# Optimization experiments

Hardware: AMD Instinct MI355X
Metric: run time of the kernel (lower is better)

The kernel has to match this reference:

```python
import math
import jax, jax.numpy as jnp
import numpy as np

IN_DIM = 512
OUT_DIM = 512
K = 3
EPS = 1e-8


def setup_inputs() -> dict:
    key = jax.random.key(0)
    k1, k2, k3 = jax.random.split(key, 3)
    b, h, w = 8, 64, 64
    x = jax.random.normal(k1, (b, IN_DIM, h, w), dtype=jnp.float32)
    style = jax.random.normal(k2, (b, IN_DIM), dtype=jnp.float32)
    weight = jax.random.normal(k3, (OUT_DIM, IN_DIM, K, K), dtype=jnp.float32)
    bias = jnp.zeros((OUT_DIM,), dtype=jnp.float32)
    return {"x": x, "style": style, "weight": weight, "bias": bias}


def _mod_weights(weight, style):
    # EqualizedWeight scaling: c = 1/sqrt(prod(shape[1:]))
    c = 1.0 / math.sqrt(IN_DIM * K * K)
    w = weight * c                                    # [out, in, k, k]
    ws = w[None] * (style[:, None, :, None, None] + 1.0)  # [b, out, in, k, k]
    sigma_inv = jax.lax.rsqrt(jnp.sum(ws * ws, axis=(2, 3, 4), keepdims=True) + EPS)
    return ws * sigma_inv


def reference(x, style, weight, bias):
    ws = _mod_weights(weight, style)                  # [b, out, in, k, k]

    def conv_one(xi, wi):
        # xi: [in, h, w], wi: [out, in, k, k]
        y = jax.lax.conv_general_dilated(
            xi[None], wi, window_strides=(1, 1), padding="SAME",
            dimension_numbers=("NCHW", "OIHW", "NCHW"))
        return y[0]

    out = jax.vmap(conv_one)(x, ws)                   # [b, out, h, w]
    return out + bias[None, :, None, None]
```

## Files before the change

### kernel.cpp

```cpp
#include <hip/hip_runtime.h>

#define CIN 512
#define COUT 512
#define HH 64
#define WW 64
#define BB 8
#define KTOT 4608

#define XPD 66
#define BUFSH (4 * 66 * 64)
#define ROWB (66 * 128)

typedef __attribute__((ext_vector_type(8))) short short8;
typedef __attribute__((ext_vector_type(4))) float f32x4;

__device__ inline unsigned short f2bf(float f) {
    unsigned int u = __float_as_uint(f);
    u += 0x7FFFu + ((u >> 16) & 1u);
    return (unsigned short)(u >> 16);
}

__device__ inline void gll16(const void* g, void* l) {
    __builtin_amdgcn_global_load_lds(
        (const __attribute__((address_space(1))) unsigned int*)g,
        (__attribute__((address_space(3))) unsigned int*)l, 16, 0, 0);
}

__global__ __launch_bounds__(256) void zring_kernel(unsigned short* __restrict__ xtp) {
    const int e = blockIdx.x * 256 + threadIdx.x;
    if (e >= BB * 260 * 64) return;
    const int unit = e & 63;
    const int sa = e >> 6;
    const int b = sa / 260;
    const int s = sa - b * 260;
    int yy, xx;
    if (s < 66)       { yy = 0;        xx = s; }
    else if (s < 132) { yy = 65;       xx = s - 66; }
    else if (s < 196) { yy = s - 131;  xx = 0; }
    else              { yy = s - 195;  xx = 65; }
    *(short8*)(xtp + ((size_t)(b * XPD + yy) * XPD + xx) * 512 + unit * 8) =
        (short8){0, 0, 0, 0, 0, 0, 0, 0};
}

__global__ __launch_bounds__(256) void xpose_kernel(const float* __restrict__ x,
                                                    const float* __restrict__ style,
                                                    unsigned short* __restrict__ xtp) {
    __shared__ float tile[32 * 65];
    __shared__ float sst[32];
    const int ic = blockIdx.x;
    const int y  = blockIdx.y;
    const int b  = blockIdx.z;
    const int t  = threadIdx.x;
    if (t < 32) sst[t] = style[b * CIN + ic * 32 + t] + 1.0f;
#pragma unroll
    for (int it = 0; it < 8; ++it) {
        int e = it * 256 + t;
        int ii = e >> 6, xx = e & 63;
        tile[ii * 65 + xx] = x[(((size_t)(b * CIN + ic * 32 + ii) * HH + y) << 6) + xx];
    }
    __syncthreads();
#pragma unroll
    for (int it = 0; it < 8; ++it) {
        int g = it * 256 + t;
        int xx = g >> 5, ii = g & 31;
        xtp[((size_t)(b * XPD + y + 1) * XPD + xx + 1) * 512 + ic * 32 + ii] =
            f2bf(tile[ii * 65 + xx] * sst[ii]);
    }
}

__global__ __launch_bounds__(256) void wpack_kernel(const float* __restrict__ weight,
                                                    unsigned short* __restrict__ wpk) {
    __shared__ float q[KTOT];
    const int o = blockIdx.x;
    const int t = threadIdx.x;
    const float* wrow = weight + (size_t)o * KTOT;
    const float cst = 1.0f / sqrtf((float)KTOT);
#pragma unroll
    for (int it = 0; it < 18; ++it) {
        int e = it * 256 + t;
        q[e] = wrow[e] * cst;
    }
    __syncthreads();
    const int g = o >> 4, l15 = o & 15;
    for (int m = t; m < 576; m += 256) {
        int c   = m / 36;
        int rem = m - c * 36;
        int tap = rem >> 2;
        int l4  = rem & 3;
        short8 v;
#pragma unroll
        for (int e = 0; e < 8; ++e)
            v[e] = (short)f2bf(q[(c * 32 + l4 * 8 + e) * 9 + tap]);
        *(short8*)(wpk + ((((size_t)c * 9 + tap) * 32 + g) * 64 + l4 * 16 + l15) * 8) = v;
    }
}

__global__ __launch_bounds__(256) void sigma_kernel(const float* __restrict__ weight,
                                                    const float* __restrict__ style,
                                                    float* __restrict__ siginv) {
    __shared__ float sred[4][8];
    const int o = blockIdx.x;
    const int t = threadIdx.x;
    const float* wrow = weight + (size_t)o * KTOT;
    float acc[8] = {0.f, 0.f, 0.f, 0.f, 0.f, 0.f, 0.f, 0.f};
#pragma unroll
    for (int ii = 0; ii < 2; ++ii) {
        const int i = t * 2 + ii;
        float wsq = 0.f;
#pragma unroll
        for (int tap = 0; tap < 9; ++tap) {
            float v = wrow[i * 9 + tap];
            wsq += v * v;
        }
#pragma unroll
        for (int b = 0; b < 8; ++b) {
            float s = style[b * CIN + i] + 1.0f;
            acc[b] += wsq * s * s;
        }
    }
#pragma unroll
    for (int b = 0; b < 8; ++b) {
        float v = acc[b];
#pragma unroll
        for (int off = 32; off > 0; off >>= 1) v += __shfl_down(v, off, 64);
        if ((t & 63) == 0) sred[t >> 6][b] = v;
    }
    __syncthreads();
    if (t < 8) {
        const float S = sred[0][t] + sred[1][t] + sred[2][t] + sred[3][t];
        siginv[t * COUT + o] = rsqrtf(S * (1.0f / (float)KTOT) + 1e-8f);
    }
}

__global__ __launch_bounds__(512, 4) void conv_kernel(const unsigned short* __restrict__ wpk,
                                                      const unsigned short* __restrict__ xtp,
                                                      const float* __restrict__ siginv,
                                                      const float* __restrict__ bias,
                                                      float* __restrict__ out) {
    __shared__ __align__(16) unsigned short xs[2 * BUFSH];
    const int bid = blockIdx.x;
    const int k  = bid & 7;
    const int tq = bid >> 3;
    const int ob = k & 1;
    const int b  = (k >> 1) * 2 + (tq >> 5);
    const int yb = tq & 31;
    const int y0 = yb * 2;

    const int tid  = threadIdx.x;
    const int lane = tid & 63;
    const int wid_u = __builtin_amdgcn_readfirstlane(tid >> 6);
    const int l15 = lane & 15, l4 = lane >> 4;
    const int og = wid_u & 3, rp = wid_u >> 2;
    const int g0 = ob * 16 + og * 4;

    const int up = lane & 7;
    const unsigned short* srcq[4];
#pragma unroll
    for (int t4 = 0; t4 < 4; ++t4) {
        const int sl = (wid_u + t4 * 8) * 8 + (lane >> 3);
        const int row = sl / 66, col = sl - row * 66;
        srcq[t4] = xtp + ((size_t)(b * XPD + y0 + row) * XPD + col) * 512 +
                   (up ^ (col & 7)) * 8;
    }
    const int col4 = 58 + (lane >> 3);
    const unsigned short* src4 =
        xtp + ((size_t)(b * XPD + y0 + 3) * XPD + col4) * 512 + (up ^ (col4 & 7)) * 8;

    int vB[3][2];
#pragma unroll
    for (int kx = 0; kx < 3; ++kx)
#pragma unroll
        for (int ks = 0; ks < 2; ++ks)
            vB[kx][ks] = (l15 + kx) * 128 + (((ks * 4 + l4) ^ ((l15 + kx) & 7)) * 16);

    f32x4 acc[4][4];
#pragma unroll
    for (int mi = 0; mi < 4; ++mi)
#pragma unroll
        for (int j = 0; j < 4; ++j) acc[mi][j] = (f32x4){0.f, 0.f, 0.f, 0.f};

    const unsigned short* wB = wpk + (size_t)g0 * 512 + lane * 8;

#define STAGE(bufp, icq)                                                                  \
    do {                                                                                  \
        unsigned short* dbase = xs + (bufp) * BUFSH + wid_u * 512;                        \
        gll16(srcq[0] + (size_t)(icq) * 64, dbase);                                       \
        gll16(srcq[1] + (size_t)(icq) * 64, dbase + 4096);                                \
        gll16(srcq[2] + (size_t)(icq) * 64, dbase + 8192);                                \
        gll16(srcq[3] + (size_t)(icq) * 64, dbase + 12288);                               \
        if (wid_u == 0)                                                                   \
            gll16(src4 + (size_t)(icq) * 64, xs + (bufp) * BUFSH + 16384);                \
    } while (0)

#define PHASE(tap, ks, wAc, cbase)                                                        \
    do {                                                                                  \
        short8 afx[4];                                                                    \
        _Pragma("unroll") for (int mi = 0; mi < 4; ++mi)                                  \
            afx[mi] = *(const short8*)((wAc) + ((ks) * 9 + (tap)) * 16384 + mi * 512);    \
        short8 bfr[4];                                                                    \
        const char* bp = (const char*)xs + (cbase) +                                      \
                         (rp + (tap) / 3) * ROWB + vB[(tap) % 3][ks];                     \
        _Pragma("unroll") for (int j = 0; j < 4; ++j)                                     \
            bfr[j] = *(const short8*)(bp + j * 2048);                                     \
        __builtin_amdgcn_s_setprio(1);                                                    \
        _Pragma("unroll") for (int mi = 0; mi < 4; ++mi)                                  \
            _Pragma("unroll") for (int j = 0; j < 4; ++j)                                 \
                acc[mi][j] = __builtin_amdgcn_mfma_f32_16x16x32_bf16(                     \
                    afx[mi], bfr[j], acc[mi][j], 0, 0, 0);                                \
        __builtin_amdgcn_s_setprio(0);                                                    \
    } while (0)

    STAGE(0, 0);
    __syncthreads();

#pragma unroll 1
    for (int ic = 0; ic < 8; ++ic) {
        if (ic < 7) STAGE((ic + 1) & 1, ic + 1);
        const unsigned short* wAc = wB + (size_t)ic * (2 * 9 * 32 * 512);
        const int cbase = (ic & 1) * (BUFSH * 2);
#pragma unroll
        for (int tap = 0; tap < 9; ++tap) {
            PHASE(tap, 0, wAc, cbase);
            PHASE(tap, 1, wAc, cbase);
        }
        __syncthreads();
    }

    const int yout = y0 + rp;
#pragma unroll
    for (int mi = 0; mi < 4; ++mi) {
        const int obase = ob * 256 + og * 64 + mi * 16 + l4 * 4;
#pragma unroll
        for (int rr = 0; rr < 4; ++rr) {
            const int o = obase + rr;
            const float sv = siginv[b * COUT + o];
            const float bv = bias[o];
            float* orow = out + (((size_t)(b * COUT + o) * HH + yout) << 6);
#pragma unroll
            for (int j = 0; j < 4; ++j) {
                orow[j * 16 + l15] = acc[mi][j][rr] * sv + bv;
            }
        }
    }
#undef STAGE
#undef PHASE
}

extern "C" void kernel_launch(void* const* d_in, const int* in_sizes, int n_in,
                              void* d_out, int out_size, void* d_ws, size_t ws_size,
                              hipStream_t stream) {
    const float* x      = (const float*)d_in[0];
    const float* style  = (const float*)d_in[1];
    const float* weight = (const float*)d_in[2];
    const float* bias   = (const float*)d_in[3];
    float* out = (float*)d_out;

    unsigned short* wpk = (unsigned short*)d_ws;
    unsigned short* xtp = wpk + (size_t)2359296;
    float* siginv = (float*)(xtp + (size_t)BB * XPD * XPD * 512);

    zring_kernel<<<520, 256, 0, stream>>>(xtp);
    xpose_kernel<<<dim3(16, HH, BB), 256, 0, stream>>>(x, style, xtp);
    wpack_kernel<<<COUT, 256, 0, stream>>>(weight, wpk);
    sigma_kernel<<<COUT, 256, 0, stream>>>(weight, style, siginv);
    conv_kernel<<<512, 512, 0, stream>>>(wpk, xtp, siginv, bias, out);
}
```

Baseline: 165.9 us.

## Shrink conv tile to one output row per block and prefetch weights two steps ahead

Each conv block now computes one output row with 4 waves instead of two rows with 8 waves. Grid size doubles to 1024 blocks and the LDS halo stage drops from 4 input rows to 3. Weight fragments are loaded into a 3-deep register ring, so A-operand global loads are issued two MFMA phases before use, hiding their latency. The trade-off is that each input row is staged 3 times instead of 2, adding LDS and global traffic. The extra register ring may also limit occupancy.

```diff
diff --git a/kernel.cpp b/kernel.cpp
--- a/kernel.cpp
+++ b/kernel.cpp
@@ -8,7 +8,7 @@
 #define KTOT 4608
 
 #define XPD 66
-#define BUFSH (4 * 66 * 64)
+#define BUFSH (3 * 66 * 64)
 #define ROWB (66 * 128)
 
 typedef __attribute__((ext_vector_type(8))) short short8;
@@ -132,7 +132,7 @@
     }
 }
 
-__global__ __launch_bounds__(512, 4) void conv_kernel(const unsigned short* __restrict__ wpk,
+__global__ __launch_bounds__(256, 3) void conv_kernel(const unsigned short* __restrict__ wpk,
                                                       const unsigned short* __restrict__ xtp,
                                                       const float* __restrict__ siginv,
                                                       const float* __restrict__ bias,
@@ -140,31 +140,30 @@
     __shared__ __align__(16) unsigned short xs[2 * BUFSH];
     const int bid = blockIdx.x;
     const int k  = bid & 7;
-    const int tq = bid >> 3;
+    const int t  = bid >> 3;
     const int ob = k & 1;
-    const int b  = (k >> 1) * 2 + (tq >> 5);
-    const int yb = tq & 31;
-    const int y0 = yb * 2;
+    const int b  = (k >> 1) * 2 + (t >> 6);
+    const int yb = t & 63;
 
     const int tid  = threadIdx.x;
     const int lane = tid & 63;
     const int wid_u = __builtin_amdgcn_readfirstlane(tid >> 6);
     const int l15 = lane & 15, l4 = lane >> 4;
-    const int og = wid_u & 3, rp = wid_u >> 2;
+    const int og = wid_u;
     const int g0 = ob * 16 + og * 4;
 
     const int up = lane & 7;
-    const unsigned short* srcq[4];
-#pragma unroll
-    for (int t4 = 0; t4 < 4; ++t4) {
-        const int sl = (wid_u + t4 * 8) * 8 + (lane >> 3);
+    const unsigned short* srcq[6];
+#pragma unroll
+    for (int tq = 0; tq < 6; ++tq) {
+        const int sl = (wid_u + tq * 4) * 8 + (lane >> 3);
         const int row = sl / 66, col = sl - row * 66;
-        srcq[t4] = xtp + ((size_t)(b * XPD + y0 + row) * XPD + col) * 512 +
+        srcq[tq] = xtp + ((size_t)(b * XPD + yb + row) * XPD + col) * 512 +
                    (up ^ (col & 7)) * 8;
     }
-    const int col4 = 58 + (lane >> 3);
-    const unsigned short* src4 =
-        xtp + ((size_t)(b * XPD + y0 + 3) * XPD + col4) * 512 + (up ^ (col4 & 7)) * 8;
+    const int col6 = 60 + (lane >> 3);
+    const unsigned short* src6 =
+        xtp + ((size_t)(b * XPD + yb + 2) * XPD + col6) * 512 + (up ^ (col6 & 7)) * 8;
 
     int vB[3][2];
 #pragma unroll
@@ -179,54 +178,63 @@
 #pragma unroll
         for (int j = 0; j < 4; ++j) acc[mi][j] = (f32x4){0.f, 0.f, 0.f, 0.f};
 
-    const unsigned short* wB = wpk + (size_t)g0 * 512 + lane * 8;
+    short8 af[3][4];
+
+    const unsigned short* aP = wpk + (size_t)g0 * 512 + lane * 8;
 
 #define STAGE(bufp, icq)                                                                  \
     do {                                                                                  \
         unsigned short* dbase = xs + (bufp) * BUFSH + wid_u * 512;                        \
-        gll16(srcq[0] + (size_t)(icq) * 64, dbase);                                       \
-        gll16(srcq[1] + (size_t)(icq) * 64, dbase + 4096);                                \
-        gll16(srcq[2] + (size_t)(icq) * 64, dbase + 8192);                                \
-        gll16(srcq[3] + (size_t)(icq) * 64, dbase + 12288);                               \
-        if (wid_u == 0)                                                                   \
-            gll16(src4 + (size_t)(icq) * 64, xs + (bufp) * BUFSH + 16384);                \
+        _Pragma("unroll") for (int tq = 0; tq < 6; ++tq)                                  \
+            gll16(srcq[tq] + (size_t)(icq) * 64, dbase + tq * 2048);                      \
+        if (wid_u == 0 && lane < 48)                                                      \
+            gll16(src6 + (size_t)(icq) * 64, xs + (bufp) * BUFSH + 12288);                \
     } while (0)
 
-#define PHASE(tap, ks, wAc, cbase)                                                        \
+#define PHASE(s, aPic, cbase)                                                             \
     do {                                                                                  \
-        short8 afx[4];                                                                    \
+        const unsigned short* pA = (aPic) + (size_t)((s) + 2) * 16384;                    \
         _Pragma("unroll") for (int mi = 0; mi < 4; ++mi)                                  \
-            afx[mi] = *(const short8*)((wAc) + ((ks) * 9 + (tap)) * 16384 + mi * 512);    \
+            af[((s) + 2) % 3][mi] = *(const short8*)(pA + mi * 512);                      \
         short8 bfr[4];                                                                    \
         const char* bp = (const char*)xs + (cbase) +                                      \
-                         (rp + (tap) / 3) * ROWB + vB[(tap) % 3][ks];                     \
+                         (((s) % 9) / 3) * ROWB + vB[((s) % 9) % 3][(s) / 9];             \
         _Pragma("unroll") for (int j = 0; j < 4; ++j)                                     \
             bfr[j] = *(const short8*)(bp + j * 2048);                                     \
         __builtin_amdgcn_s_setprio(1);                                                    \
         _Pragma("unroll") for (int mi = 0; mi < 4; ++mi)                                  \
             _Pragma("unroll") for (int j = 0; j < 4; ++j)                                 \
                 acc[mi][j] = __builtin_amdgcn_mfma_f32_16x16x32_bf16(                     \
-                    afx[mi], bfr[j], acc[mi][j], 0, 0, 0);                                \
+                    af[(s) % 3][mi], bfr[j], acc[mi][j], 0, 0, 0);                        \
         __builtin_amdgcn_s_setprio(0);                                                    \
     } while (0)
 
+    af[0][0] = *(const short8*)(aP + 0 * 512);
+    af[0][1] = *(const short8*)(aP + 1 * 512);
+    af[0][2] = *(const short8*)(aP + 2 * 512);
+    af[0][3] = *(const short8*)(aP + 3 * 512);
+    {
+        const unsigned short* p1 = aP + 16384;
+        af[1][0] = *(const short8*)(p1 + 0 * 512);
+        af[1][1] = *(const short8*)(p1 + 1 * 512);
+        af[1][2] = *(const short8*)(p1 + 2 * 512);
+        af[1][3] = *(const short8*)(p1 + 3 * 512);
+    }
     STAGE(0, 0);
     __syncthreads();
 
 #pragma unroll 1
     for (int ic = 0; ic < 8; ++ic) {
         if (ic < 7) STAGE((ic + 1) & 1, ic + 1);
-        const unsigned short* wAc = wB + (size_t)ic * (2 * 9 * 32 * 512);
+        const unsigned short* aPic = aP + (size_t)ic * (18 * 16384);
         const int cbase = (ic & 1) * (BUFSH * 2);
 #pragma unroll
-        for (int tap = 0; tap < 9; ++tap) {
-            PHASE(tap, 0, wAc, cbase);
-            PHASE(tap, 1, wAc, cbase);
+        for (int s = 0; s < 18; ++s) {
+            PHASE(s, aPic, cbase);
         }
         __syncthreads();
     }
 
-    const int yout = y0 + rp;
 #pragma unroll
     for (int mi = 0; mi < 4; ++mi) {
         const int obase = ob * 256 + og * 64 + mi * 16 + l4 * 4;
@@ -235,7 +243,7 @@
             const int o = obase + rr;
             const float sv = siginv[b * COUT + o];
             const float bv = bias[o];
-            float* orow = out + (((size_t)(b * COUT + o) * HH + yout) << 6);
+            float* orow = out + (((size_t)(b * COUT + o) * HH + yb) << 6);
 #pragma unroll
             for (int j = 0; j < 4; ++j) {
                 orow[j * 16 + l15] = acc[mi][j][rr] * sv + bv;
@@ -263,5 +271,5 @@
     xpose_kernel<<<dim3(16, HH, BB), 256, 0, stream>>>(x, style, xtp);
     wpack_kernel<<<COUT, 256, 0, stream>>>(weight, wpk);
     sigma_kernel<<<COUT, 256, 0, stream>>>(weight, style, siginv);
-    conv_kernel<<<512, 512, 0, stream>>>(wpk, xtp, siginv, bias, out);
-}
+    conv_kernel<<<1024, 256, 0, stream>>>(wpk, xtp, siginv, bias, out);
+}
```

Result: no change. 168.7 us (+1.6%).

## Enlarge conv tile to 8 rows by 128 channels with register-rotated weight prefetch

Applied to the files above, without the earlier changes.

Reshapes the conv block tile from 2 output rows × 256 output channels to 8 rows × 128 channels, with 32-channel staging chunks over 16 iterations. Each wave now holds 4×8 accumulators, and weight fragments are prefetched two taps ahead through a three-slot register rotation. The grid drops to 256 blocks at occupancy 2. The aim is more weight reuse per loaded fragment, less redundant halo loading, and hiding global weight-load latency behind MFMAs. The cost is more register pressure and only one block per CU, so less latency hiding across blocks.

```diff
diff --git a/kernel.cpp b/kernel.cpp
--- a/kernel.cpp
+++ b/kernel.cpp
@@ -8,8 +8,9 @@
 #define KTOT 4608
 
 #define XPD 66
-#define BUFSH (4 * 66 * 64)
-#define ROWB (66 * 128)
+#define BUFSH (10 * 66 * 32)
+#define BUFB  (BUFSH * 2)
+#define ROWB  (66 * 64)
 
 typedef __attribute__((ext_vector_type(8))) short short8;
 typedef __attribute__((ext_vector_type(4))) float f32x4;
@@ -132,7 +133,7 @@
     }
 }
 
-__global__ __launch_bounds__(512, 4) void conv_kernel(const unsigned short* __restrict__ wpk,
+__global__ __launch_bounds__(512, 2) void conv_kernel(const unsigned short* __restrict__ wpk,
                                                       const unsigned short* __restrict__ xtp,
                                                       const float* __restrict__ siginv,
                                                       const float* __restrict__ bias,
@@ -140,110 +141,124 @@
     __shared__ __align__(16) unsigned short xs[2 * BUFSH];
     const int bid = blockIdx.x;
     const int k  = bid & 7;
-    const int tq = bid >> 3;
-    const int ob = k & 1;
-    const int b  = (k >> 1) * 2 + (tq >> 5);
-    const int yb = tq & 31;
-    const int y0 = yb * 2;
+    const int t  = bid >> 3;
+    const int ob = k & 3;
+    const int b  = (k >> 2) * 4 + (t >> 3);
+    const int rg = t & 7;
+    const int y0r = rg * 8;
 
     const int tid  = threadIdx.x;
     const int lane = tid & 63;
     const int wid_u = __builtin_amdgcn_readfirstlane(tid >> 6);
     const int l15 = lane & 15, l4 = lane >> 4;
-    const int og = wid_u & 3, rp = wid_u >> 2;
-    const int g0 = ob * 16 + og * 4;
-
-    const int up = lane & 7;
-    const unsigned short* srcq[4];
-#pragma unroll
-    for (int t4 = 0; t4 < 4; ++t4) {
-        const int sl = (wid_u + t4 * 8) * 8 + (lane >> 3);
+    const int og = wid_u & 1, rp = wid_u >> 1;
+    const int g0 = ob * 8 + og * 4;
+
+    const int u = lane & 3;
+    const unsigned short* srcq[5];
+#pragma unroll
+    for (int t4 = 0; t4 < 5; ++t4) {
+        const int sl = (wid_u + t4 * 8) * 16 + (lane >> 2);
         const int row = sl / 66, col = sl - row * 66;
-        srcq[t4] = xtp + ((size_t)(b * XPD + y0 + row) * XPD + col) * 512 +
-                   (up ^ (col & 7)) * 8;
-    }
-    const int col4 = 58 + (lane >> 3);
-    const unsigned short* src4 =
-        xtp + ((size_t)(b * XPD + y0 + 3) * XPD + col4) * 512 + (up ^ (col4 & 7)) * 8;
-
-    int vB[3][2];
+        srcq[t4] = xtp + ((size_t)(b * XPD + y0r + row) * XPD + col) * 512 +
+                   (u ^ ((col >> 1) & 3)) * 8;
+    }
+    const unsigned short* srcX = xtp;
+    if (wid_u <= 1) {
+        const int sl = (40 + wid_u) * 16 + (lane >> 2);
+        const int row = sl / 66, col = sl - row * 66;
+        const int rowc = (row < 10) ? row : 9;
+        srcX = xtp + ((size_t)(b * XPD + y0r + rowc) * XPD + col) * 512 +
+               (u ^ ((col >> 1) & 3)) * 8;
+    }
+
+    const char* vBp[3];
 #pragma unroll
     for (int kx = 0; kx < 3; ++kx)
-#pragma unroll
-        for (int ks = 0; ks < 2; ++ks)
-            vB[kx][ks] = (l15 + kx) * 128 + (((ks * 4 + l4) ^ ((l15 + kx) & 7)) * 16);
-
-    f32x4 acc[4][4];
+        vBp[kx] = (const char*)xs + rp * (2 * ROWB) + (l15 + kx) * 64 +
+                  ((l4 ^ (((l15 + kx) >> 1) & 3)) * 16);
+
+    f32x4 acc[4][8];
 #pragma unroll
     for (int mi = 0; mi < 4; ++mi)
 #pragma unroll
-        for (int j = 0; j < 4; ++j) acc[mi][j] = (f32x4){0.f, 0.f, 0.f, 0.f};
-
-    const unsigned short* wB = wpk + (size_t)g0 * 512 + lane * 8;
+        for (int j = 0; j < 8; ++j) acc[mi][j] = (f32x4){0.f, 0.f, 0.f, 0.f};
+
+    short8 af[3][4];
+
+    const unsigned short* aP = wpk + (size_t)g0 * 512 + lane * 8;
 
 #define STAGE(bufp, icq)                                                                  \
     do {                                                                                  \
-        unsigned short* dbase = xs + (bufp) * BUFSH + wid_u * 512;                        \
-        gll16(srcq[0] + (size_t)(icq) * 64, dbase);                                       \
-        gll16(srcq[1] + (size_t)(icq) * 64, dbase + 4096);                                \
-        gll16(srcq[2] + (size_t)(icq) * 64, dbase + 8192);                                \
-        gll16(srcq[3] + (size_t)(icq) * 64, dbase + 12288);                               \
+        unsigned short* db = xs + (bufp) * BUFSH;                                         \
+        _Pragma("unroll") for (int t4 = 0; t4 < 5; ++t4)                                  \
+            gll16(srcq[t4] + (size_t)(icq) * 32, db + (wid_u + t4 * 8) * 512);            \
         if (wid_u == 0)                                                                   \
-            gll16(src4 + (size_t)(icq) * 64, xs + (bufp) * BUFSH + 16384);                \
+            gll16(srcX + (size_t)(icq) * 32, db + 40 * 512);                              \
+        else if (wid_u == 1 && lane < 16)                                                 \
+            gll16(srcX + (size_t)(icq) * 32, db + 41 * 512);                              \
     } while (0)
 
-#define PHASE(tap, ks, wAc, cbase)                                                        \
+#define TAPPHASE(tp, P, aIC)                                                              \
     do {                                                                                  \
-        short8 afx[4];                                                                    \
+        const unsigned short* pA = (aIC) + (size_t)((tp) + 2) * 16384;                    \
         _Pragma("unroll") for (int mi = 0; mi < 4; ++mi)                                  \
-            afx[mi] = *(const short8*)((wAc) + ((ks) * 9 + (tap)) * 16384 + mi * 512);    \
-        short8 bfr[4];                                                                    \
-        const char* bp = (const char*)xs + (cbase) +                                      \
-                         (rp + (tap) / 3) * ROWB + vB[(tap) % 3][ks];                     \
-        _Pragma("unroll") for (int j = 0; j < 4; ++j)                                     \
-            bfr[j] = *(const short8*)(bp + j * 2048);                                     \
+            af[((tp) + 2) % 3][mi] = *(const short8*)(pA + mi * 512);                     \
+        short8 bfr[8];                                                                    \
+        _Pragma("unroll") for (int j = 0; j < 8; ++j)                                     \
+            bfr[j] = *(const short8*)(vBp[(tp) % 3] + (P) * BUFB +                        \
+                ((tp) / 3 + (j >> 2)) * ROWB + (j & 3) * 1024);                           \
         __builtin_amdgcn_s_setprio(1);                                                    \
         _Pragma("unroll") for (int mi = 0; mi < 4; ++mi)                                  \
-            _Pragma("unroll") for (int j = 0; j < 4; ++j)                                 \
+            _Pragma("unroll") for (int j = 0; j < 8; ++j)                                 \
                 acc[mi][j] = __builtin_amdgcn_mfma_f32_16x16x32_bf16(                     \
-                    afx[mi], bfr[j], acc[mi][j], 0, 0, 0);                                \
+                    af[(tp) % 3][mi], bfr[j], acc[mi][j], 0, 0, 0);                       \
         __builtin_amdgcn_s_setprio(0);                                                    \
     } while (0)
 
+#define ICBODY(icv, P)                                                                    \
+    do {                                                                                  \
+        if ((icv) < 15) STAGE((P) ^ 1, (icv) + 1);                                        \
+        const unsigned short* aIC = aP + (size_t)(icv) * (9 * 16384);                     \
+        TAPPHASE(0, P, aIC); TAPPHASE(1, P, aIC); TAPPHASE(2, P, aIC);                    \
+        TAPPHASE(3, P, aIC); TAPPHASE(4, P, aIC); TAPPHASE(5, P, aIC);                    \
+        TAPPHASE(6, P, aIC); TAPPHASE(7, P, aIC); TAPPHASE(8, P, aIC);                    \
+        __syncthreads();                                                                  \
+    } while (0)
+
+#pragma unroll
+    for (int mi = 0; mi < 4; ++mi) af[0][mi] = *(const short8*)(aP + mi * 512);
+#pragma unroll
+    for (int mi = 0; mi < 4; ++mi) af[1][mi] = *(const short8*)(aP + 16384 + mi * 512);
     STAGE(0, 0);
     __syncthreads();
 
 #pragma unroll 1
-    for (int ic = 0; ic < 8; ++ic) {
-        if (ic < 7) STAGE((ic + 1) & 1, ic + 1);
-        const unsigned short* wAc = wB + (size_t)ic * (2 * 9 * 32 * 512);
-        const int cbase = (ic & 1) * (BUFSH * 2);
-#pragma unroll
-        for (int tap = 0; tap < 9; ++tap) {
-            PHASE(tap, 0, wAc, cbase);
-            PHASE(tap, 1, wAc, cbase);
-        }
-        __syncthreads();
-    }
-
-    const int yout = y0 + rp;
+    for (int ic = 0; ic < 16; ic += 2) {
+        ICBODY(ic, 0);
+        ICBODY(ic + 1, 1);
+    }
+
+    const int yb0 = y0r + rp * 2;
 #pragma unroll
     for (int mi = 0; mi < 4; ++mi) {
-        const int obase = ob * 256 + og * 64 + mi * 16 + l4 * 4;
+        const int obase = ob * 128 + og * 64 + mi * 16 + l4 * 4;
 #pragma unroll
         for (int rr = 0; rr < 4; ++rr) {
             const int o = obase + rr;
             const float sv = siginv[b * COUT + o];
             const float bv = bias[o];
-            float* orow = out + (((size_t)(b * COUT + o) * HH + yout) << 6);
-#pragma unroll
-            for (int j = 0; j < 4; ++j) {
-                orow[j * 16 + l15] = acc[mi][j][rr] * sv + bv;
+#pragma unroll
+            for (int j = 0; j < 8; ++j) {
+                const int yout = yb0 + (j >> 2);
+                out[(((size_t)(b * COUT + o) * HH + yout) << 6) + (j & 3) * 16 + l15] =
+                    acc[mi][j][rr] * sv + bv;
             }
         }
     }
 #undef STAGE
-#undef PHASE
+#undef TAPPHASE
+#undef ICBODY
 }
 
 extern "C" void kernel_launch(void* const* d_in, const int* in_sizes, int n_in,
@@ -263,5 +278,5 @@
     xpose_kernel<<<dim3(16, HH, BB), 256, 0, stream>>>(x, style, xtp);
     wpack_kernel<<<COUT, 256, 0, stream>>>(weight, wpk);
     sigma_kernel<<<COUT, 256, 0, stream>>>(weight, style, siginv);
-    conv_kernel<<<512, 512, 0, stream>>>(wpk, xtp, siginv, bias, out);
-}
+    conv_kernel<<<256, 512, 0, stream>>>(wpk, xtp, siginv, bias, out);
+}
```

New measurement: 167.0 us. Within noise of the previous version (+0.6%).
